# Performance work log

Measured on AMD Instinct MI355X. Metric: run time of the kernel, lower is better.

The kernel has to match this reference:

```python
import jax, jax.numpy as jnp
import numpy as np

M = 8      # number of modalities (len(ModalityType))
D = 256    # embedding_dim
B = 8192   # batch size


def setup_inputs() -> dict:
    key = jax.random.key(0)
    ks = jax.random.split(key, 12)
    s = 1.0 / np.sqrt(D)
    x = jax.random.normal(ks[0], (M, B, D), dtype=jnp.float32)
    reasoning_query = jax.random.normal(ks[1], (B, D), dtype=jnp.float32)
    # Per ordered modality pair (src, tgt): seq_len=1 MHA reduces to out_proj(V_proj(tgt)).
    Wv = jax.random.normal(ks[2], (M, M, D, D), dtype=jnp.float32) * s
    bv = jnp.zeros((M, M, D), dtype=jnp.float32)
    Wo = jax.random.normal(ks[3], (M, M, D, D), dtype=jnp.float32) * s
    bo = jnp.zeros((M, M, D), dtype=jnp.float32)
    # Per-modality fusion MLP: Linear(2D->D), ReLU, Linear(D->D)  (dropout = eval/identity)
    W1 = jax.random.normal(ks[4], (M, D, 2 * D), dtype=jnp.float32) * s
    b1 = jnp.zeros((M, D), dtype=jnp.float32)
    W2 = jax.random.normal(ks[5], (M, D, D), dtype=jnp.float32) * s
    b2 = jnp.zeros((M, D), dtype=jnp.float32)
    # Attention controller: Linear(2D->D), ReLU, Linear(D->1), Sigmoid
    Wc1 = jax.random.normal(ks[6], (D, 2 * D), dtype=jnp.float32) * s
    bc1 = jnp.zeros((D,), dtype=jnp.float32)
    wc2 = jax.random.normal(ks[7], (D,), dtype=jnp.float32) * s
    bc2 = jnp.zeros((1,), dtype=jnp.float32)
    return dict(x=x, reasoning_query=reasoning_query, Wv=Wv, bv=bv, Wo=Wo, bo=bo,
                W1=W1, b1=b1, W2=W2, b2=b2, Wc1=Wc1, bc1=bc1, wc2=wc2, bc2=bc2)


def reference(x, reasoning_query, Wv, bv, Wo, bo, W1, b1, W2, b2, Wc1, bc1, wc2, bc2):
    m = x.shape[0]
    # Cross-modal attention with seq_len=1: softmax over one key == 1, so the
    # attended output is exactly out_proj(V_proj(tgt_embedding)) for every pair.
    h = jnp.einsum('tbd,sted->stbe', x, Wv) + bv[:, :, None, :]          # [M,M,B,D]
    ctx = jnp.einsum('stbe,stoe->stbo', h, Wo) + bo[:, :, None, :]       # [M,M,B,D]
    # Mean over the M-1 target modalities (src != tgt), matching stack(...).mean(-1)
    offdiag = (1.0 - jnp.eye(m, dtype=x.dtype))[:, :, None, None]
    cross = (ctx * offdiag).sum(axis=1) / (m - 1)                         # [M,B,D]
    # Per-modality fusion MLP on cat([original, cross])
    comb = jnp.concatenate([x, cross], axis=-1)                           # [M,B,2D]
    hid = jax.nn.relu(jnp.einsum('mbf,mdf->mbd', comb, W1) + b1[:, None, :])
    fused = jnp.einsum('mbd,mod->mbo', hid, W2) + b2[:, None, :]          # [M,B,D]
    # Reasoning-query gating controller
    q = jnp.broadcast_to(reasoning_query[None], fused.shape)              # [M,B,D]
    qc = jnp.concatenate([q, fused], axis=-1)                             # [M,B,2D]
    ch = jax.nn.relu(jnp.einsum('mbf,df->mbd', qc, Wc1) + bc1)
    score = jax.nn.sigmoid(jnp.einsum('mbd,d->mb', ch, wc2) + bc2)        # [M,B]
    gated = fused * score[..., None]
    unified = gated.mean(axis=0)                                          # [B,D]
    return unified
```

## Files before the change

kernel.cpp:

```cpp
#include <hip/hip_runtime.h>

#define MMOD 8
#define BB 8192
#define DD 256

typedef unsigned short u16;
typedef __attribute__((ext_vector_type(8))) short s16x8;
typedef __attribute__((ext_vector_type(4))) float f32x4;
typedef __attribute__((ext_vector_type(8))) unsigned short u16x8;

typedef __attribute__((address_space(3))) unsigned short lds_u16;
typedef __attribute__((address_space(1))) const unsigned short gl_u16;

__device__ __forceinline__ float b2f(u16 u){ union{unsigned i; float f;} x; x.i=((unsigned)u)<<16; return x.f; }
__device__ __forceinline__ u16 f2b(float f){ union{float f; unsigned i;} x; x.f=f; unsigned r = x.i + 0x7FFF + ((x.i>>16)&1u); return (u16)(r>>16); }

__device__ __forceinline__ void async_cp16(const u16* g, u16* l){
  __builtin_amdgcn_global_load_lds((gl_u16*)g, (lds_u16*)l, 16, 0, 0);
}

struct ConvArgs {
  const float* src[10];
  u16*         dst[10];
  int          n[10];
};
__global__ void convert_kernel(ConvArgs a){
  const long long stride = (long long)gridDim.x * blockDim.x;
  const long long base   = (long long)blockIdx.x * blockDim.x + threadIdx.x;
  for (int s = 0; s < 10; s++){
    const int n  = a.n[s];
    const int n8 = n >> 3;
    const float* sp = a.src[s];
    u16* dst = a.dst[s];
    for (long long i = base; i < n8; i += stride){
      float4 lo = ((const float4*)sp)[i*2];
      float4 hi = ((const float4*)sp)[i*2+1];
      u16x8 p;
      p[0]=f2b(lo.x); p[1]=f2b(lo.y); p[2]=f2b(lo.z); p[3]=f2b(lo.w);
      p[4]=f2b(hi.x); p[5]=f2b(hi.y); p[6]=f2b(hi.z); p[7]=f2b(hi.w);
      *(u16x8*)(dst + (i<<3)) = p;
    }
    for (long long i = ((long long)n8<<3) + base; i < n; i += stride)
      dst[i] = f2b(sp[i]);
  }
}

__device__ __forceinline__ s16x8 load8_f32(const float* p, long long idx){
  float4 lo = *(const float4*)(p + idx);
  float4 hi = *(const float4*)(p + idx + 4);
  s16x8 r;
  r[0]=(short)f2b(lo.x); r[1]=(short)f2b(lo.y); r[2]=(short)f2b(lo.z); r[3]=(short)f2b(lo.w);
  r[4]=(short)f2b(hi.x); r[5]=(short)f2b(hi.y); r[6]=(short)f2b(hi.z); r[7]=(short)f2b(hi.w);
  return r;
}

struct GArgs {
  const u16* A;  long long a_z; long long a_piece; int lda;
  const u16* A2; long long a2_z;
  const u16* B;  long long b_z; int ldb;
  u16*       C;  long long c_z; long long c_npiece; int ldc;
  const u16* bias; long long bias_z;
  const float* cbias;
  const u16* addm;
  const u16* wc2;
  float*     scores;
  float scale;
  int K;
  int relu;
};

__global__ __launch_bounds__(256, 2) void gemm_bt(GArgs g){
  alignas(16) __shared__ u16 lA[128*64];
  alignas(16) __shared__ u16 lB[128*64];
  const int tid  = threadIdx.x;
  const int lane = tid & 63;
  const int w    = tid >> 6;
  const int z    = blockIdx.z;

  const u16* Bbase = g.B + (long long)z * g.b_z + (long long)(blockIdx.y * 128) * g.ldb;

  f32x4 acc[4][4];
  #pragma unroll
  for (int i=0;i<4;i++)
    #pragma unroll
    for (int j=0;j<4;j++)
      #pragma unroll
      for (int r=0;r<4;r++) acc[i][j][r] = 0.0f;

  const int wr = (w >> 1) * 64, wc = (w & 1) * 64;
  const int fm = lane & 15;
  const int fk = (lane >> 4) * 8;
  const long long arow0 = (long long)blockIdx.x * 128;

  const int sr = lane >> 3;
  const int sq = (lane & 7) ^ sr;

  for (int k0 = 0; k0 < g.K; k0 += 64){
    const u16* Abase0 = (g.A2 && k0 >= 256) ? (g.A2 + (long long)z * g.a2_z)
                                            : (g.A  + (long long)z * g.a_z);
    const u16* At = Abase0 + (long long)(k0 >> 8) * g.a_piece + (k0 & 255);
    const u16* Bt = Bbase + k0;
    __syncthreads();
    #pragma unroll
    for (int i=0;i<4;i++){
      int r = i*32 + w*8 + sr;
      async_cp16(At + (arow0 + r) * (long long)g.lda + sq*8, lA + (i*256 + w*64) * 8);
      async_cp16(Bt + (long long)r * g.ldb + sq*8, lB + (i*256 + w*64) * 8);
    }
    __syncthreads();
    #pragma unroll
    for (int kk = 0; kk < 64; kk += 32){
      s16x8 af[4], bfr[4];
      const int qf = (kk + fk) >> 3;
      #pragma unroll
      for (int mi=0; mi<4; mi++){
        int r = wr + mi*16 + fm;
        af[mi] = *(const s16x8*)(lA + (r*8 + (qf ^ (r & 7))) * 8);
      }
      #pragma unroll
      for (int ni=0; ni<4; ni++){
        int r = wc + ni*16 + fm;
        bfr[ni] = *(const s16x8*)(lB + (r*8 + (qf ^ (r & 7))) * 8);
      }
      #pragma unroll
      for (int mi=0; mi<4; mi++)
        #pragma unroll
        for (int ni=0; ni<4; ni++)
          acc[mi][ni] = __builtin_amdgcn_mfma_f32_16x16x32_bf16(af[mi], bfr[ni], acc[mi][ni], 0, 0, 0);
    }
  }

  u16* Cb = g.C + (long long)z * g.c_z;
  const u16* biasp = g.bias ? g.bias + (long long)z * g.bias_z : (const u16*)0;
  #pragma unroll
  for (int mi=0; mi<4; mi++){
    #pragma unroll
    for (int ni=0; ni<4; ni++){
      int n = blockIdx.y*128 + wc + ni*16 + fm;
      float bb = 0.0f;
      if (g.cbias) bb = g.cbias[n];
      else if (biasp) bb = b2f(biasp[n]);
      long long cn = ((long long)(n >> 8)) * g.c_npiece + (n & 255);
      #pragma unroll
      for (int r=0; r<4; r++){
        long long b = arow0 + wr + mi*16 + (lane>>4)*4 + r;
        float v = acc[mi][ni][r] * g.scale + bb;
        if (g.addm) v += b2f(g.addm[b*256 + n]);
        if (g.relu) v = v > 0.0f ? v : 0.0f;
        Cb[cn + b * (long long)g.ldc] = f2b(v);
      }
    }
  }
}

__global__ __launch_bounds__(512, 2) void gemm_8ph(GArgs g){
  alignas(16) __shared__ u16 L[65536];
  const int tid  = threadIdx.x;
  const int lane = tid & 63;
  const int w    = tid >> 6;
  const int z    = blockIdx.z;

  const int wr  = w >> 2;
  const int wcn = w & 3;
  const int fm  = lane & 15;
  const int fq  = lane >> 4;

  const long long arow0 = (long long)blockIdx.x * 256;
  const long long nrow0 = (long long)blockIdx.y * 256;

  const int r0  = tid >> 3;
  const int r1  = r0 + 64;
  const int cs  = tid & 7;
  const int gc0 = cs ^ (r0 & 7);
  const int gc1 = cs ^ (r1 & 7);
  const int ldst0 = (w * 64) * 8;
  const int ldst1 = (512 + w * 64) * 8;

  const u16* Az = g.A + (long long)z * g.a_z;
  const u16* Bz = g.B + (long long)z * g.b_z;

#define STAGE_A8(c, k0s, h) do{ \
    const u16* gb_ = Az + (long long)((k0s) >> 8) * g.a_piece + ((k0s) & 255); \
    const long long gr_ = arow0 + (h) * 128; \
    u16* lb_ = L + ((c) * 2 + 0) * 16384 + (h) * 8192; \
    async_cp16(gb_ + (gr_ + r0) * (long long)g.lda + gc0 * 8, lb_ + ldst0); \
    async_cp16(gb_ + (gr_ + r1) * (long long)g.lda + gc1 * 8, lb_ + ldst1); \
  }while(0)
#define STAGE_B8(c, k0s, h) do{ \
    const u16* gb_ = Bz + (k0s); \
    const long long gr_ = nrow0 + (h) * 128; \
    u16* lb_ = L + ((c) * 2 + 1) * 16384 + (h) * 8192; \
    async_cp16(gb_ + (gr_ + r0) * (long long)g.ldb + gc0 * 8, lb_ + ldst0); \
    async_cp16(gb_ + (gr_ + r1) * (long long)g.ldb + gc1 * 8, lb_ + ldst1); \
  }while(0)

  f32x4 acc[8][4];
  #pragma unroll
  for (int i=0;i<8;i++)
    #pragma unroll
    for (int j=0;j<4;j++)
      #pragma unroll
      for (int r=0;r<4;r++) acc[i][j][r] = 0.0f;

  const int T = g.K >> 6;

  STAGE_A8(0, 0, 0);  STAGE_A8(0, 0, 1);
  STAGE_B8(0, 0, 0);  STAGE_B8(0, 0, 1);
  STAGE_B8(1, 64, 0); STAGE_B8(1, 64, 1);
  asm volatile("s_waitcnt vmcnt(4)" ::: "memory");
  __builtin_amdgcn_s_barrier();

  int c = 0;
  for (int t = 0; t < T; ++t, c ^= 1){
    const int k0 = t << 6;
    const u16* lA = L + (c * 2 + 0) * 16384;
    const u16* lB = L + (c * 2 + 1) * 16384;
    s16x8 bf[4][2];
    #pragma unroll
    for (int q = 0; q < 4; ++q){
      if (q == 0 && t + 1 < T) STAGE_A8(c ^ 1, k0 + 64, 0);
      if (q == 1 && t + 1 < T) STAGE_A8(c ^ 1, k0 + 64, 1);
      if (q == 2 && t + 2 < T) STAGE_B8(c,     k0 + 128, 0);
      if (q == 3 && t + 2 < T) STAGE_B8(c,     k0 + 128, 1);
      if (q == 0){
        #pragma unroll
        for (int ni = 0; ni < 4; ni++){
          const int R = wcn * 64 + ni * 16 + fm;
          #pragma unroll
          for (int kk = 0; kk < 2; kk++){
            const int qf = kk * 4 + fq;
            bf[ni][kk] = *(const s16x8*)(lB + R * 64 + ((qf ^ (R & 7)) << 3));
          }
        }
      }
      s16x8 af[2][2];
      #pragma unroll
      for (int j = 0; j < 2; j++){
        const int R = wr * 128 + (q * 2 + j) * 16 + fm;
        #pragma unroll
        for (int kk = 0; kk < 2; kk++){
          const int qf = kk * 4 + fq;
          af[j][kk] = *(const s16x8*)(lA + R * 64 + ((qf ^ (R & 7)) << 3));
        }
      }
      __builtin_amdgcn_s_barrier();
      __builtin_amdgcn_s_setprio(1);
      #pragma unroll
      for (int kk = 0; kk < 2; kk++)
        #pragma unroll
        for (int j = 0; j < 2; j++)
          #pragma unroll
          for (int ni = 0; ni < 4; ni++)
            acc[q*2+j][ni] = __builtin_amdgcn_mfma_f32_16x16x32_bf16(af[j][kk], bf[ni][kk], acc[q*2+j][ni], 0, 0, 0);
      __builtin_amdgcn_s_setprio(0);
      if (q == 3){
        if (t + 2 < T)      asm volatile("s_waitcnt vmcnt(4)" ::: "memory");
        else if (t + 1 < T) asm volatile("s_waitcnt vmcnt(0)" ::: "memory");
      }
      __builtin_amdgcn_s_barrier();
    }
  }

  u16* Cb = g.C + (long long)z * g.c_z;
  const u16* biasp = g.bias ? g.bias + (long long)z * g.bias_z : (const u16*)0;
  #pragma unroll
  for (int mi = 0; mi < 8; mi++){
    #pragma unroll
    for (int ni = 0; ni < 4; ni++){
      const int n = (int)nrow0 + wcn * 64 + ni * 16 + fm;
      float bb = 0.0f;
      if (g.cbias) bb = g.cbias[n];
      else if (biasp) bb = b2f(biasp[n]);
      const long long cn = ((long long)(n >> 8)) * g.c_npiece + (n & 255);
      #pragma unroll
      for (int r = 0; r < 4; r++){
        const long long b = arow0 + wr * 128 + mi * 16 + fq * 4 + r;
        float v = acc[mi][ni][r] * g.scale + bb;
        if (g.relu) v = v > 0.0f ? v : 0.0f;
        Cb[cn + b * (long long)g.ldc] = f2b(v);
      }
    }
  }
#undef STAGE_A8
#undef STAGE_B8
}

__global__ __launch_bounds__(256, 4) void gemm_thin(GArgs g){
  alignas(16) __shared__ u16 lA[64*64];
  alignas(16) __shared__ u16 lB[256*64];
  const int tid  = threadIdx.x;
  const int lane = tid & 63;
  const int w    = tid >> 6;
  const int z    = blockIdx.z;

  const u16* Bbase = g.B + (long long)z * g.b_z;

  f32x4 acc[16];
  #pragma unroll
  for (int j=0;j<16;j++)
    #pragma unroll
    for (int r=0;r<4;r++) acc[j][r] = 0.0f;

  const int fm = lane & 15;
  const int fk = (lane >> 4) * 8;
  const long long arow0 = (long long)blockIdx.x * 64;

  const int sr = lane >> 3;
  const int sq = (lane & 7) ^ sr;

  for (int k0 = 0; k0 < g.K; k0 += 64){
    const u16* Abase0 = (g.A2 && k0 >= 256) ? (g.A2 + (long long)z * g.a2_z)
                                            : (g.A  + (long long)z * g.a_z);
    const u16* At = Abase0 + (long long)(k0 >> 8) * g.a_piece + (k0 & 255);
    const u16* Bt = Bbase + k0;
    __syncthreads();
    #pragma unroll
    for (int i=0;i<2;i++){
      int r = i*32 + w*8 + sr;
      async_cp16(At + (arow0 + r) * (long long)g.lda + sq*8, lA + (i*256 + w*64) * 8);
    }
    #pragma unroll
    for (int i=0;i<8;i++){
      int r = i*32 + w*8 + sr;
      async_cp16(Bt + (long long)r * g.ldb + sq*8, lB + (i*256 + w*64) * 8);
    }
    __syncthreads();
    #pragma unroll
    for (int kk = 0; kk < 64; kk += 32){
      const int qf = (kk + fk) >> 3;
      int ra = w*16 + fm;
      s16x8 af = *(const s16x8*)(lA + (ra*8 + (qf ^ (ra & 7))) * 8);
      #pragma unroll
      for (int ni=0; ni<16; ni++){
        int r = ni*16 + fm;
        s16x8 bfr = *(const s16x8*)(lB + (r*8 + (qf ^ (r & 7))) * 8);
        acc[ni] = __builtin_amdgcn_mfma_f32_16x16x32_bf16(af, bfr, acc[ni], 0, 0, 0);
      }
    }
  }

  u16* Cb = g.C + (long long)z * g.c_z;
  const u16* biasp = g.bias ? g.bias + (long long)z * g.bias_z : (const u16*)0;
  #pragma unroll
  for (int ni=0; ni<16; ni++){
    int n = ni*16 + fm;
    float bb = 0.0f;
    if (g.cbias) bb = g.cbias[n];
    else if (biasp) bb = b2f(biasp[n]);
    #pragma unroll
    for (int r=0; r<4; r++){
      long long b = arow0 + w*16 + (lane>>4)*4 + r;
      float v = acc[ni][r] * g.scale + bb;
      if (g.addm) v += b2f(g.addm[b*256 + n]);
      if (g.relu) v = v > 0.0f ? v : 0.0f;
      Cb[b * (long long)g.ldc + n] = f2b(v);
    }
  }
}

__global__ __launch_bounds__(256, 4) void gemm_score(GArgs g){
  alignas(16) __shared__ u16 lA[64*64];
  alignas(16) __shared__ u16 lB[256*64];
  const int tid  = threadIdx.x;
  const int lane = tid & 63;
  const int w    = tid >> 6;
  const int z    = blockIdx.z;

  const u16* Bbase = g.B;

  f32x4 acc[16];
  #pragma unroll
  for (int j=0;j<16;j++)
    #pragma unroll
    for (int r=0;r<4;r++) acc[j][r] = 0.0f;

  const int fm = lane & 15;
  const int fk = (lane >> 4) * 8;
  const long long arow0 = (long long)blockIdx.x * 64;

  const int sr = lane >> 3;
  const int sq = (lane & 7) ^ sr;

  for (int k0 = 0; k0 < g.K; k0 += 64){
    const u16* At = g.A + (long long)z * g.a_z + k0;
    const u16* Bt = Bbase + k0;
    __syncthreads();
    #pragma unroll
    for (int i=0;i<2;i++){
      int r = i*32 + w*8 + sr;
      async_cp16(At + (arow0 + r) * (long long)g.lda + sq*8, lA + (i*256 + w*64) * 8);
    }
    #pragma unroll
    for (int i=0;i<8;i++){
      int r = i*32 + w*8 + sr;
      async_cp16(Bt + (long long)r * g.ldb + sq*8, lB + (i*256 + w*64) * 8);
    }
    __syncthreads();
    #pragma unroll
    for (int kk = 0; kk < 64; kk += 32){
      const int qf = (kk + fk) >> 3;
      int ra = w*16 + fm;
      s16x8 af = *(const s16x8*)(lA + (ra*8 + (qf ^ (ra & 7))) * 8);
      #pragma unroll
      for (int ni=0; ni<16; ni++){
        int r = ni*16 + fm;
        s16x8 bfr = *(const s16x8*)(lB + (r*8 + (qf ^ (r & 7))) * 8);
        acc[ni] = __builtin_amdgcn_mfma_f32_16x16x32_bf16(af, bfr, acc[ni], 0, 0, 0);
      }
    }
  }

  float p[4] = {0.f, 0.f, 0.f, 0.f};
  #pragma unroll
  for (int ni=0; ni<16; ni++){
    int n = ni*16 + fm;
    float bb = b2f(g.bias[n]);
    float wcv = b2f(g.wc2[n]);
    #pragma unroll
    for (int r=0; r<4; r++){
      long long b = arow0 + w*16 + (lane>>4)*4 + r;
      float v = acc[ni][r] + bb + b2f(g.addm[b*256 + n]);
      v = v > 0.0f ? v : 0.0f;
      p[r] += v * wcv;
    }
  }
  #pragma unroll
  for (int r=0; r<4; r++){
    #pragma unroll
    for (int off=1; off<16; off<<=1) p[r] += __shfl_xor(p[r], off);
  }
  if (fm == 0){
    float bc2f = g.cbias[0];
    #pragma unroll
    for (int r=0; r<4; r++){
      long long b = arow0 + w*16 + (lane>>4)*4 + r;
      g.scores[(long long)z*BB + b] = 1.0f / (1.0f + __expf(-(p[r] + bc2f)));
    }
  }
}

__global__ __launch_bounds__(256, 2) void build_wb(const float* Wo, const float* Wv, u16* WB){
  alignas(16) __shared__ u16 lA[128*64];
  alignas(16) __shared__ u16 lB[128*64];
  const int tid  = threadIdx.x;
  const int lane = tid & 63;
  const int w    = tid >> 6;
  const int z = blockIdx.z, s = z >> 3, t = z & 7;
  const long long zoff = (long long)z * 65536;

  f32x4 acc[4][4];
  #pragma unroll
  for (int i=0;i<4;i++)
    #pragma unroll
    for (int j=0;j<4;j++)
      #pragma unroll
      for (int r=0;r<4;r++) acc[i][j][r] = 0.0f;

  const int wr = (w >> 1) * 64, wc = (w & 1) * 64;
  const int fm = lane & 15;
  const int fk = (lane >> 4) * 8;

  int srow[4], sq[4];
  #pragma unroll
  for (int i=0;i<4;i++){
    int c = i*256 + tid;
    srow[i] = c >> 3;
    sq[i]   = (c & 7) ^ (srow[i] & 7);
  }

  for (int k0 = 0; k0 < 256; k0 += 64){
    s16x8 va[4], vt[4];
    #pragma unroll
    for (int i=0;i<4;i++){
      long long aidx = zoff + (long long)(blockIdx.x*128 + srow[i]) * 256 + k0 + sq[i]*8;
      va[i] = load8_f32(Wo, aidx);
    }
    #pragma unroll
    for (int j=0;j<4;j++){
      int id = j*256 + tid;
      int e  = id >> 4;
      int dc = (id & 15) * 8;
      long long bidx = zoff + (long long)(k0 + e) * 256 + blockIdx.y*128 + dc;
      vt[j] = load8_f32(Wv, bidx);
    }
    __syncthreads();
    #pragma unroll
    for (int i=0;i<4;i++){
      int c = i*256 + tid;
      *(s16x8*)(lA + c*8) = va[i];
    }
    #pragma unroll
    for (int j=0;j<4;j++){
      int id = j*256 + tid;
      int e  = id >> 4;
      int dc = (id & 15) * 8;
      #pragma unroll
      for (int u=0; u<8; u++){
        int d = dc + u;
        lB[(d*8 + ((e>>3) ^ (d & 7)))*8 + (e & 7)] = (u16)vt[j][u];
      }
    }
    __syncthreads();
    #pragma unroll
    for (int kk = 0; kk < 64; kk += 32){
      s16x8 af[4], bfr[4];
      const int qf = (kk + fk) >> 3;
      #pragma unroll
      for (int mi=0; mi<4; mi++){
        int r = wr + mi*16 + fm;
        af[mi] = *(const s16x8*)(lA + (r*8 + (qf ^ (r & 7))) * 8);
      }
      #pragma unroll
      for (int ni=0; ni<4; ni++){
        int r = wc + ni*16 + fm;
        bfr[ni] = *(const s16x8*)(lB + (r*8 + (qf ^ (r & 7))) * 8);
      }
      #pragma unroll
      for (int mi=0; mi<4; mi++)
        #pragma unroll
        for (int ni=0; ni<4; ni++)
          acc[mi][ni] = __builtin_amdgcn_mfma_f32_16x16x32_bf16(af[mi], bfr[ni], acc[mi][ni], 0, 0, 0);
    }
    __syncthreads();
  }
  const int diag = (s == t);
  #pragma unroll
  for (int mi=0; mi<4; mi++){
    #pragma unroll
    for (int ni=0; ni<4; ni++){
      int d = blockIdx.y*128 + wc + ni*16 + fm;
      #pragma unroll
      for (int r=0; r<4; r++){
        int o = blockIdx.x*128 + wr + mi*16 + (lane>>4)*4 + r;
        float v = diag ? 0.0f : acc[mi][ni][r];
        WB[(long long)(s*256 + o) * 2048 + t*256 + d] = f2b(v);
      }
    }
  }
}

__global__ __launch_bounds__(256) void cb_kernel(const float* bv, const float* Wo, const float* bo, float* cb){
  int z = blockIdx.x, s = z >> 3, t = z & 7;
  if (s == t) return;
  int lane = threadIdx.x & 63, w = threadIdx.x >> 6;
  float4 bvv = *(const float4*)(bv + (long long)z*256 + lane*4);
  #pragma unroll
  for (int i=0; i<16; i++){
    int row = blockIdx.y*64 + w*16 + i;
    float4 wv4 = *(const float4*)(Wo + (long long)z*65536 + (long long)row*256 + lane*4);
    float p = wv4.x*bvv.x + wv4.y*bvv.y + wv4.z*bvv.z + wv4.w*bvv.w;
    #pragma unroll
    for (int off=32; off>0; off>>=1) p += __shfl_xor(p, off);
    if (lane == 0)
      atomicAdd(&cb[s*256 + row], (p + bo[(long long)z*256 + row]) * (1.0f/7.0f));
  }
}

__global__ __launch_bounds__(256) void final_gate(const u16* fused, const float* scores, float* out){
  int b = blockIdx.x;
  int tid = threadIdx.x;
  float sc[8];
  #pragma unroll
  for (int m=0; m<8; m++) sc[m] = scores[(long long)m*BB + b];
  float acc = 0.0f;
  #pragma unroll
  for (int m=0; m<8; m++)
    acc += b2f(fused[((long long)m*BB + b)*256 + tid]) * sc[m];
  out[(long long)b*256 + tid] = acc * 0.125f;
}

extern "C" void kernel_launch(void* const* d_in, const int* in_sizes, int n_in,
                              void* d_out, int out_size, void* d_ws, size_t ws_size,
                              hipStream_t stream){
  const float* x   = (const float*)d_in[0];
  const float* q   = (const float*)d_in[1];
  const float* Wv  = (const float*)d_in[2];
  const float* bv  = (const float*)d_in[3];
  const float* Wo  = (const float*)d_in[4];
  const float* bo  = (const float*)d_in[5];
  const float* W1  = (const float*)d_in[6];
  const float* b1  = (const float*)d_in[7];
  const float* W2  = (const float*)d_in[8];
  const float* b2  = (const float*)d_in[9];
  const float* Wc1 = (const float*)d_in[10];
  const float* bc1 = (const float*)d_in[11];
  const float* wc2 = (const float*)d_in[12];
  const float* bc2 = (const float*)d_in[13];

  char* ws = (char*)d_ws;
  u16*   xb    = (u16*)(ws + 0LL);
  u16*   qb    = (u16*)(ws + 33554432LL);
  u16*   cross = (u16*)(ws + 37748736LL);
  u16*   hid   = (u16*)(ws + 71303168LL);
  u16*   WB    = (u16*)(ws + 104857600LL);
  u16*   W1b   = (u16*)(ws + 113246208LL);
  u16*   W2b   = (u16*)(ws + 115343360LL);
  u16*   Wc1b  = (u16*)(ws + 116391936LL);
  u16*   b1b   = (u16*)(ws + 116654080LL);
  u16*   b2b   = (u16*)(ws + 116658176LL);
  u16*   bc1b  = (u16*)(ws + 116662272LL);
  u16*   wc2b  = (u16*)(ws + 116662784LL);
  float* bc2f  = (float*)(ws + 116663296LL);
  float* cb    = (float*)(ws + 116663424LL);
  u16*   fused = xb;
  u16*   qctx  = WB;
  float* scores = (float*)(ws + 104857600LL + 4194304LL);

  ConvArgs ca{};
  ca.src[0]=x;   ca.dst[0]=xb;   ca.n[0]=MMOD*BB*DD;
  ca.src[1]=q;   ca.dst[1]=qb;   ca.n[1]=BB*DD;
  ca.src[2]=W1;  ca.dst[2]=W1b;  ca.n[2]=MMOD*DD*2*DD;
  ca.src[3]=W2;  ca.dst[3]=W2b;  ca.n[3]=MMOD*DD*DD;
  ca.src[4]=Wc1; ca.dst[4]=Wc1b; ca.n[4]=DD*2*DD;
  ca.src[5]=b1;  ca.dst[5]=b1b;  ca.n[5]=MMOD*DD;
  ca.src[6]=b2;  ca.dst[6]=b2b;  ca.n[6]=MMOD*DD;
  ca.src[7]=bc1; ca.dst[7]=bc1b; ca.n[7]=DD;
  ca.src[8]=wc2; ca.dst[8]=wc2b; ca.n[8]=DD;
  ca.src[9]=bc2; ca.dst[9]=bc1b; ca.n[9]=0;
  convert_kernel<<<1024, 256, 0, stream>>>(ca);
  hipMemcpyAsync(bc2f, bc2, sizeof(float), hipMemcpyDeviceToDevice, stream);

  hipMemsetAsync(cb, 0, 2048*sizeof(float), stream);
  build_wb<<<dim3(2,2,64), 256, 0, stream>>>(Wo, Wv, WB);
  cb_kernel<<<dim3(64,4), 256, 0, stream>>>(bv, Wo, bo, cb);

  const long long BD = (long long)BB * DD;

  GArgs g2{};
  g2.A = xb; g2.a_z = 0; g2.a_piece = BD; g2.lda = 256; g2.A2 = 0; g2.a2_z = 0;
  g2.B = WB; g2.b_z = 0; g2.ldb = 2048;
  g2.C = cross; g2.c_z = 0; g2.c_npiece = BD; g2.ldc = 256;
  g2.bias = 0; g2.bias_z = 0; g2.cbias = cb; g2.addm = 0; g2.wc2 = 0; g2.scores = 0;
  g2.scale = 1.0f/7.0f; g2.K = 2048; g2.relu = 0;
  gemm_8ph<<<dim3(32,8,1), 512, 0, stream>>>(g2);

  GArgs g5a{};
  g5a.A = qb; g5a.a_z = 0; g5a.a_piece = 0; g5a.lda = 256; g5a.A2 = 0; g5a.a2_z = 0;
  g5a.B = Wc1b; g5a.b_z = 0; g5a.ldb = 512;
  g5a.C = qctx; g5a.c_z = 0; g5a.c_npiece = 0; g5a.ldc = 256;
  g5a.bias = 0; g5a.bias_z = 0; g5a.cbias = 0; g5a.addm = 0; g5a.wc2 = 0; g5a.scores = 0;
  g5a.scale = 1.0f; g5a.K = 256; g5a.relu = 0;
  gemm_thin<<<dim3(128,1,1), 256, 0, stream>>>(g5a);

  GArgs g3{};
  g3.A = xb; g3.a_z = BD; g3.a_piece = 0; g3.lda = 256; g3.A2 = cross; g3.a2_z = BD;
  g3.B = W1b; g3.b_z = (long long)DD*2*DD; g3.ldb = 512;
  g3.C = hid; g3.c_z = BD; g3.c_npiece = 0; g3.ldc = 256;
  g3.bias = b1b; g3.bias_z = 256; g3.cbias = 0; g3.addm = 0; g3.wc2 = 0; g3.scores = 0;
  g3.scale = 1.0f; g3.K = 512; g3.relu = 1;
  gemm_thin<<<dim3(128,1,8), 256, 0, stream>>>(g3);

  GArgs g4{};
  g4.A = hid; g4.a_z = BD; g4.a_piece = 0; g4.lda = 256; g4.A2 = 0; g4.a2_z = 0;
  g4.B = W2b; g4.b_z = (long long)DD*DD; g4.ldb = 256;
  g4.C = fused; g4.c_z = BD; g4.c_npiece = 0; g4.ldc = 256;
  g4.bias = b2b; g4.bias_z = 256; g4.cbias = 0; g4.addm = 0; g4.wc2 = 0; g4.scores = 0;
  g4.scale = 1.0f; g4.K = 256; g4.relu = 0;
  gemm_thin<<<dim3(128,1,8), 256, 0, stream>>>(g4);

  GArgs g5b{};
  g5b.A = fused; g5b.a_z = BD; g5b.a_piece = 0; g5b.lda = 256; g5b.A2 = 0; g5b.a2_z = 0;
  g5b.B = Wc1b + 256; g5b.b_z = 0; g5b.ldb = 512;
  g5b.C = 0; g5b.c_z = 0; g5b.c_npiece = 0; g5b.ldc = 0;
  g5b.bias = bc1b; g5b.bias_z = 0; g5b.cbias = bc2f; g5b.addm = qctx;
  g5b.wc2 = wc2b; g5b.scores = scores;
  g5b.scale = 1.0f; g5b.K = 256; g5b.relu = 1;
  gemm_score<<<dim3(128,1,8), 256, 0, stream>>>(g5b);

  final_gate<<<dim3(BB), 256, 0, stream>>>(fused, scores, (float*)d_out);

  (void)in_sizes; (void)n_in; (void)out_size; (void)ws_size;
}
```

Measured before the change: 364.6 us.

## Fuse fusion-MLP GEMMs into one kernel keeping hidden activations in LDS

Replaces the two separate gemm_thin launches for the fusion MLP (Linear 2D->D with ReLU, then Linear D->D) with a single kernel. Each block computes a 64-row hidden tile, applies bias and ReLU, and stores it swizzled in LDS. The second GEMM then reads that tile directly, so the hidden tensor never goes out to global memory and back and one launch is dropped. The cost is 64KB of LDS per block, which limits occupancy, and a grid of 128x8 blocks each with 64 rows; the unused gemm_bt kernel is also removed.

```diff
diff --git a/kernel.cpp b/kernel.cpp
--- a/kernel.cpp
+++ b/kernel.cpp
@@ -8,6 +8,8 @@
 typedef __attribute__((ext_vector_type(8))) short s16x8;
 typedef __attribute__((ext_vector_type(4))) float f32x4;
 typedef __attribute__((ext_vector_type(8))) unsigned short u16x8;
+typedef __attribute__((ext_vector_type(4))) unsigned short u16x4;
+typedef __attribute__((ext_vector_type(4))) short s16x4;
 
 typedef __attribute__((address_space(3))) unsigned short lds_u16;
 typedef __attribute__((address_space(1))) const unsigned short gl_u16;
@@ -69,90 +71,6 @@
   int relu;
 };
 
-__global__ __launch_bounds__(256, 2) void gemm_bt(GArgs g){
-  alignas(16) __shared__ u16 lA[128*64];
-  alignas(16) __shared__ u16 lB[128*64];
-  const int tid  = threadIdx.x;
-  const int lane = tid & 63;
-  const int w    = tid >> 6;
-  const int z    = blockIdx.z;
-
-  const u16* Bbase = g.B + (long long)z * g.b_z + (long long)(blockIdx.y * 128) * g.ldb;
-
-  f32x4 acc[4][4];
-  #pragma unroll
-  for (int i=0;i<4;i++)
-    #pragma unroll
-    for (int j=0;j<4;j++)
-      #pragma unroll
-      for (int r=0;r<4;r++) acc[i][j][r] = 0.0f;
-
-  const int wr = (w >> 1) * 64, wc = (w & 1) * 64;
-  const int fm = lane & 15;
-  const int fk = (lane >> 4) * 8;
-  const long long arow0 = (long long)blockIdx.x * 128;
-
-  const int sr = lane >> 3;
-  const int sq = (lane & 7) ^ sr;
-
-  for (int k0 = 0; k0 < g.K; k0 += 64){
-    const u16* Abase0 = (g.A2 && k0 >= 256) ? (g.A2 + (long long)z * g.a2_z)
-                                            : (g.A  + (long long)z * g.a_z);
-    const u16* At = Abase0 + (long long)(k0 >> 8) * g.a_piece + (k0 & 255);
-    const u16* Bt = Bbase + k0;
-    __syncthreads();
-    #pragma unroll
-    for (int i=0;i<4;i++){
-      int r = i*32 + w*8 + sr;
-      async_cp16(At + (arow0 + r) * (long long)g.lda + sq*8, lA + (i*256 + w*64) * 8);
-      async_cp16(Bt + (long long)r * g.ldb + sq*8, lB + (i*256 + w*64) * 8);
-    }
-    __syncthreads();
-    #pragma unroll
-    for (int kk = 0; kk < 64; kk += 32){
-      s16x8 af[4], bfr[4];
-      const int qf = (kk + fk) >> 3;
-      #pragma unroll
-      for (int mi=0; mi<4; mi++){
-        int r = wr + mi*16 + fm;
-        af[mi] = *(const s16x8*)(lA + (r*8 + (qf ^ (r & 7))) * 8);
-      }
-      #pragma unroll
-      for (int ni=0; ni<4; ni++){
-        int r = wc + ni*16 + fm;
-        bfr[ni] = *(const s16x8*)(lB + (r*8 + (qf ^ (r & 7))) * 8);
-      }
-      #pragma unroll
-      for (int mi=0; mi<4; mi++)
-        #pragma unroll
-        for (int ni=0; ni<4; ni++)
-          acc[mi][ni] = __builtin_amdgcn_mfma_f32_16x16x32_bf16(af[mi], bfr[ni], acc[mi][ni], 0, 0, 0);
-    }
-  }
-
-  u16* Cb = g.C + (long long)z * g.c_z;
-  const u16* biasp = g.bias ? g.bias + (long long)z * g.bias_z : (const u16*)0;
-  #pragma unroll
-  for (int mi=0; mi<4; mi++){
-    #pragma unroll
-    for (int ni=0; ni<4; ni++){
-      int n = blockIdx.y*128 + wc + ni*16 + fm;
-      float bb = 0.0f;
-      if (g.cbias) bb = g.cbias[n];
-      else if (biasp) bb = b2f(biasp[n]);
-      long long cn = ((long long)(n >> 8)) * g.c_npiece + (n & 255);
-      #pragma unroll
-      for (int r=0; r<4; r++){
-        long long b = arow0 + wr + mi*16 + (lane>>4)*4 + r;
-        float v = acc[mi][ni][r] * g.scale + bb;
-        if (g.addm) v += b2f(g.addm[b*256 + n]);
-        if (g.relu) v = v > 0.0f ? v : 0.0f;
-        Cb[cn + b * (long long)g.ldc] = f2b(v);
-      }
-    }
-  }
-}
-
 __global__ __launch_bounds__(512, 2) void gemm_8ph(GArgs g){
   alignas(16) __shared__ u16 L[65536];
   const int tid  = threadIdx.x;
@@ -354,6 +272,137 @@
       if (g.addm) v += b2f(g.addm[b*256 + n]);
       if (g.relu) v = v > 0.0f ? v : 0.0f;
       Cb[b * (long long)g.ldc + n] = f2b(v);
+    }
+  }
+}
+
+struct S34Args {
+  const u16* X;
+  const u16* CR;
+  const u16* W1;
+  const u16* W2;
+  const u16* b1;
+  const u16* b2;
+  u16*       F;
+};
+__global__ __launch_bounds__(256, 2) void gemm_s34(S34Args a){
+  alignas(16) __shared__ u16 lB[256*64];
+  alignas(16) __shared__ u16 lH[64*256];
+  u16* lA = lH;
+
+  const int tid  = threadIdx.x;
+  const int lane = tid & 63;
+  const int w    = tid >> 6;
+  const int z    = blockIdx.z;
+
+  const int fm = lane & 15;
+  const int fq = lane >> 4;
+  const long long arow0 = (long long)blockIdx.x * 64;
+  const long long BD = (long long)BB * DD;
+
+  const int sr = lane >> 3;
+  const int sq = (lane & 7) ^ sr;
+
+  const u16* Xz  = a.X  + (long long)z * BD;
+  const u16* CRz = a.CR + (long long)z * BD;
+  const u16* W1z = a.W1 + (long long)z * 131072;
+  const u16* W2z = a.W2 + (long long)z * 65536;
+
+  f32x4 acc[16];
+  #pragma unroll
+  for (int j=0;j<16;j++)
+    #pragma unroll
+    for (int r=0;r<4;r++) acc[j][r] = 0.0f;
+
+  for (int k0 = 0; k0 < 512; k0 += 64){
+    const u16* At = (k0 < 256) ? (Xz + k0) : (CRz + (k0 - 256));
+    const u16* Bt = W1z + k0;
+    __syncthreads();
+    #pragma unroll
+    for (int i=0;i<2;i++){
+      int r = i*32 + w*8 + sr;
+      async_cp16(At + (arow0 + r) * 256 + sq*8, lA + (i*256 + w*64) * 8);
+    }
+    #pragma unroll
+    for (int i=0;i<8;i++){
+      int r = i*32 + w*8 + sr;
+      async_cp16(Bt + (long long)r * 512 + sq*8, lB + (i*256 + w*64) * 8);
+    }
+    __syncthreads();
+    #pragma unroll
+    for (int kk = 0; kk < 64; kk += 32){
+      const int qf = (kk >> 3) + fq;
+      int ra = w*16 + fm;
+      s16x8 af = *(const s16x8*)(lA + (ra*8 + (qf ^ (ra & 7))) * 8);
+      #pragma unroll
+      for (int ni=0; ni<16; ni++){
+        int r = ni*16 + fm;
+        s16x8 bfr = *(const s16x8*)(lB + (r*8 + (qf ^ (r & 7))) * 8);
+        acc[ni] = __builtin_amdgcn_mfma_f32_16x16x32_bf16(bfr, af, acc[ni], 0, 0, 0);
+      }
+    }
+  }
+
+  __syncthreads();
+
+  {
+    const int b = w*16 + fm;
+    #pragma unroll
+    for (int ni=0; ni<16; ni++){
+      s16x4 b1v = *(const s16x4*)(a.b1 + (long long)z*256 + ni*16 + fq*4);
+      u16x4 pk;
+      #pragma unroll
+      for (int r=0; r<4; r++){
+        float v = acc[ni][r] + b2f((u16)b1v[r]);
+        v = v > 0.0f ? v : 0.0f;
+        pk[r] = f2b(v);
+      }
+      const int c = ni*2 + (fq >> 1);
+      const int csw = (c & ~7) | ((c & 7) ^ (b & 7));
+      *(u16x4*)(lH + b*256 + csw*8 + (fq & 1)*4) = pk;
+    }
+  }
+
+  f32x4 acc2[16];
+  #pragma unroll
+  for (int j=0;j<16;j++)
+    #pragma unroll
+    for (int r=0;r<4;r++) acc2[j][r] = 0.0f;
+
+  for (int k0 = 0; k0 < 256; k0 += 64){
+    const u16* Bt = W2z + k0;
+    __syncthreads();
+    #pragma unroll
+    for (int i=0;i<8;i++){
+      int r = i*32 + w*8 + sr;
+      async_cp16(Bt + (long long)r * 256 + sq*8, lB + (i*256 + w*64) * 8);
+    }
+    __syncthreads();
+    #pragma unroll
+    for (int kk = 0; kk < 64; kk += 32){
+      const int ra = w*16 + fm;
+      const int qa = ((k0 + kk) >> 3) + fq;
+      const int qsw = (qa & ~7) | ((qa & 7) ^ (ra & 7));
+      s16x8 af = *(const s16x8*)(lH + ra*256 + qsw*8);
+      const int qf = (kk >> 3) + fq;
+      #pragma unroll
+      for (int ni=0; ni<16; ni++){
+        int r = ni*16 + fm;
+        s16x8 bfr = *(const s16x8*)(lB + (r*8 + (qf ^ (r & 7))) * 8);
+        acc2[ni] = __builtin_amdgcn_mfma_f32_16x16x32_bf16(af, bfr, acc2[ni], 0, 0, 0);
+      }
+    }
+  }
+
+  u16* Fz = a.F + (long long)z * BD;
+  #pragma unroll
+  for (int ni=0; ni<16; ni++){
+    int o = ni*16 + fm;
+    float bb = b2f(a.b2[(long long)z*256 + o]);
+    #pragma unroll
+    for (int r=0; r<4; r++){
+      long long b = arow0 + w*16 + fq*4 + r;
+      Fz[b * 256 + o] = f2b(acc2[ni][r] + bb);
     }
   }
 }
@@ -591,7 +640,6 @@
   u16*   xb    = (u16*)(ws + 0LL);
   u16*   qb    = (u16*)(ws + 33554432LL);
   u16*   cross = (u16*)(ws + 37748736LL);
-  u16*   hid   = (u16*)(ws + 71303168LL);
   u16*   WB    = (u16*)(ws + 104857600LL);
   u16*   W1b   = (u16*)(ws + 113246208LL);
   u16*   W2b   = (u16*)(ws + 115343360LL);
@@ -642,21 +690,10 @@
   g5a.scale = 1.0f; g5a.K = 256; g5a.relu = 0;
   gemm_thin<<<dim3(128,1,1), 256, 0, stream>>>(g5a);
 
-  GArgs g3{};
-  g3.A = xb; g3.a_z = BD; g3.a_piece = 0; g3.lda = 256; g3.A2 = cross; g3.a2_z = BD;
-  g3.B = W1b; g3.b_z = (long long)DD*2*DD; g3.ldb = 512;
-  g3.C = hid; g3.c_z = BD; g3.c_npiece = 0; g3.ldc = 256;
-  g3.bias = b1b; g3.bias_z = 256; g3.cbias = 0; g3.addm = 0; g3.wc2 = 0; g3.scores = 0;
-  g3.scale = 1.0f; g3.K = 512; g3.relu = 1;
-  gemm_thin<<<dim3(128,1,8), 256, 0, stream>>>(g3);
-
-  GArgs g4{};
-  g4.A = hid; g4.a_z = BD; g4.a_piece = 0; g4.lda = 256; g4.A2 = 0; g4.a2_z = 0;
-  g4.B = W2b; g4.b_z = (long long)DD*DD; g4.ldb = 256;
-  g4.C = fused; g4.c_z = BD; g4.c_npiece = 0; g4.ldc = 256;
-  g4.bias = b2b; g4.bias_z = 256; g4.cbias = 0; g4.addm = 0; g4.wc2 = 0; g4.scores = 0;
-  g4.scale = 1.0f; g4.K = 256; g4.relu = 0;
-  gemm_thin<<<dim3(128,1,8), 256, 0, stream>>>(g4);
+  S34Args s34{};
+  s34.X = xb; s34.CR = cross; s34.W1 = W1b; s34.W2 = W2b;
+  s34.b1 = b1b; s34.b2 = b2b; s34.F = fused;
+  gemm_s34<<<dim3(128,1,8), 256, 0, stream>>>(s34);
 
   GArgs g5b{};
   g5b.A = fused; g5b.a_z = BD; g5b.a_piece = 0; g5b.lda = 256; g5b.A2 = 0; g5b.a2_z = 0;
```

Result: faster. 349.6 us (-4.1%).
